# Kernel optimization log

Measured on AMD Instinct MI355X. Metric: run time of the kernel, lower is better.

Reference implementation:

```python
import jax, jax.numpy as jnp
import numpy as np

GAMMA = 1.0
T = 2.0
EPS = 1e-8

def setup_inputs() -> dict:
    key = jax.random.key(0)
    k1, k2 = jax.random.split(key)
    N, D = 8192, 64
    user_vecs = jax.random.normal(k1, (N, D), dtype=jnp.float32)
    item_vecs = jax.random.normal(k2, (N, D), dtype=jnp.float32)
    return {"user_vecs": user_vecs, "item_vecs": item_vecs}

def _normalize(x):
    return x / jnp.linalg.norm(x, axis=-1, keepdims=True)

def _alignment(u, i):
    u = _normalize(u)
    i = _normalize(i)
    return jnp.mean(jnp.sum((u - i) ** 2, axis=1))

def _uniformity(x):
    # log( mean_{i<j} exp(-t * ||x_i - x_j||^2) + eps ) with normalized x.
    # For unit vectors ||x_i - x_j||^2 = 2 - 2 <x_i, x_j>. Use full symmetric
    # Gram matrix: sum over off-diagonal = 2 * sum over i<j; diag contributes
    # exp(0) = 1 per row, so subtract N, divide by N*(N-1).
    x = _normalize(x)
    n = x.shape[0]
    gram = x @ x.T                       # [N, N]
    sq_pdist = jnp.maximum(2.0 - 2.0 * gram, 0.0)
    total = jnp.sum(jnp.exp(-T * sq_pdist))
    mean_pair = (total - n) / (n * (n - 1))
    return jnp.log(mean_pair + EPS)

def reference(user_vecs, item_vecs):
    align = _alignment(user_vecs, item_vecs)
    uniform = GAMMA * (_uniformity(user_vecs) + _uniformity(item_vecs)) / 2.0
    return align + uniform
```

## Files before the change

kernel.cpp:

```cpp
#include <hip/hip_runtime.h>
#include <cstdint>


#define NROWS 8192
#define DIM 64
#define NT2 32
#define GRAM_SLOTS (NT2 * (NT2 + 1))
#define K1_BLOCKS 512

static constexpr float SQRT_SCALE = 2.4022448309943147f;
static constexpr float E4        = 54.598150033144236f;
static constexpr float E4_INV    = 0.018315638888734179f;
static constexpr float EPS_F = 1e-8f;

typedef __bf16 bf16x8 __attribute__((ext_vector_type(8)));
typedef float f32x4 __attribute__((ext_vector_type(4)));

__device__ __forceinline__ unsigned short f32_to_bf16_rn(float f) {
    union { float f; uint32_t u; } c; c.f = f;
    uint32_t u = c.u;
    uint32_t r = u + 0x7FFFu + ((u >> 16) & 1u);
    return (unsigned short)(r >> 16);
}

__global__ void __launch_bounds__(256) normalize_align_kernel(
    const float* __restrict__ user, const float* __restrict__ item,
    unsigned short* __restrict__ xu, unsigned short* __restrict__ xi,
    float* __restrict__ pa, float* __restrict__ acc, unsigned* __restrict__ ctr)
{
    if (blockIdx.x == 0) {
        if (threadIdx.x < 16) acc[threadIdx.x] = 0.0f;
        else if (threadIdx.x == 16) *ctr = 0u;
    }

    const int wave = threadIdx.x >> 6;
    const int lane = threadIdx.x & 63;
    const int wid  = blockIdx.x * 4 + wave;

    float asum = 0.0f;
    #pragma unroll
    for (int r = 0; r < 4; ++r) {
        const int idx = (wid * 4 + r) * DIM + lane;
        float u = user[idx];
        float v = item[idx];
        float su = u * u, sv = v * v;
        #pragma unroll
        for (int m = 1; m < 64; m <<= 1) {
            su += __shfl_xor(su, m, 64);
            sv += __shfl_xor(sv, m, 64);
        }
        float iu = rsqrtf(su); iu = iu * (1.5f - 0.5f * su * iu * iu);
        float iv = rsqrtf(sv); iv = iv * (1.5f - 0.5f * sv * iv * iv);
        float un = u * iu, vn = v * iv;
        xu[idx] = f32_to_bf16_rn(un * SQRT_SCALE);
        xi[idx] = f32_to_bf16_rn(vn * SQRT_SCALE);
        float d = un - vn;
        asum += d * d;
    }
    #pragma unroll
    for (int m = 1; m < 64; m <<= 1) asum += __shfl_xor(asum, m, 64);
    __shared__ float ws4[4];
    if (lane == 0) ws4[wave] = asum;
    __syncthreads();
    if (threadIdx.x == 0) pa[blockIdx.x] = ws4[0] + ws4[1] + ws4[2] + ws4[3];
}

__global__ void __launch_bounds__(512, 8) gram_exp_kernel(
    const unsigned short* __restrict__ xu,
    const unsigned short* __restrict__ xi,
    const float* __restrict__ pa,
    float* __restrict__ acc, unsigned* __restrict__ ctr,
    float* __restrict__ out)
{
    const int bx = blockIdx.x, by = blockIdx.y;
    const unsigned short* __restrict__ X;
    int bi, bj;
    bool is_item;
    if (by < NT2) {
        if (by >= bx) { X = xu; bi = bx; bj = by; is_item = false; }
        else          { X = xi; bi = by; bj = bx; is_item = true;  }
    } else            { X = xi; bi = bx; bj = bx; is_item = true;  }
    const bool diag = (bi == bj);

    __shared__ unsigned short lds[16384];
    __shared__ float wsum[8];
    __shared__ float fin[16];
    __shared__ bool amLast;

    const int wave = threadIdx.x >> 6;
    const int lane = threadIdx.x & 63;

    bf16x8 a[2][2];
    {
        const int arow = bi * 256 + wave * 32 + (lane & 15);
        const int acol = (lane >> 4) * 8;
        #pragma unroll
        for (int rb = 0; rb < 2; ++rb)
            #pragma unroll
            for (int ks = 0; ks < 2; ++ks)
                a[rb][ks] = *reinterpret_cast<const bf16x8*>(
                    X + (arow + rb * 16) * DIM + acol + ks * 32);
    }

    {
        const int base = bj * 256;
        #pragma unroll
        for (int i = 0; i < 4; ++i) {
            int n = i * 512 + threadIdx.x;
            int r = n >> 3, c = n & 7;
            bf16x8 v = *reinterpret_cast<const bf16x8*>(X + (base + r) * DIM + c * 8);
            int di = (r >> 4) * 1024 + c * 128 + (r & 15) * 8;
            *reinterpret_cast<bf16x8*>(&lds[di]) = v;
        }
    }
    __syncthreads();

    float l0 = 0.0f, l1 = 0.0f;
    #pragma unroll 2
    for (int cb = 0; cb < 16; ++cb) {
        bf16x8 b0 = *reinterpret_cast<const bf16x8*>(&lds[cb * 1024 + lane * 8]);
        bf16x8 b1 = *reinterpret_cast<const bf16x8*>(&lds[cb * 1024 + 512 + lane * 8]);
        #pragma unroll
        for (int rb = 0; rb < 2; ++rb) {
            f32x4 c = {0.f, 0.f, 0.f, 0.f};
            c = __builtin_amdgcn_mfma_f32_16x16x32_bf16(a[rb][0], b0, c, 0, 0, 0);
            c = __builtin_amdgcn_mfma_f32_16x16x32_bf16(a[rb][1], b1, c, 0, 0, 0);
            #pragma unroll
            for (int e = 0; e < 4; ++e) {
                float ex = __builtin_amdgcn_exp2f(c[e]);
                if (diag) ex = fminf(ex, E4);
                if (e & 1) l1 += ex; else l0 += ex;
            }
        }
    }

    float local = l0 + l1;
    #pragma unroll
    for (int m = 1; m < 64; m <<= 1) local += __shfl_xor(local, m, 64);
    if (lane == 0) wsum[wave] = local;
    __syncthreads();
    if (threadIdx.x == 0) {
        float t = 0.f;
        #pragma unroll
        for (int w = 0; w < 8; ++w) t += wsum[w];
        t = diag ? t : 2.0f * t;
        atomicAdd(&acc[(is_item ? 8 : 0) + (bx & 7)], t);
        __threadfence();
        unsigned prev = atomicAdd(ctr, 1u);
        amLast = (prev == GRAM_SLOTS - 1);
    }
    __syncthreads();

    if (amLast) {
        __threadfence();
        float av = pa[threadIdx.x];
        #pragma unroll
        for (int m = 1; m < 64; m <<= 1) av += __shfl_xor(av, m, 64);
        if (lane == 0) wsum[wave] = av;
        if (threadIdx.x < 16)
            fin[threadIdx.x] = atomicAdd(&acc[threadIdx.x], 0.0f);
        __syncthreads();
        if (threadIdx.x == 0) {
            float A = 0.f;
            #pragma unroll
            for (int w = 0; w < 8; ++w) A += wsum[w];
            float su = 0.f, si = 0.f;
            #pragma unroll
            for (int s = 0; s < 8; ++s) { su += fin[s]; si += fin[8 + s]; }
            su *= E4_INV; si *= E4_INV;
            const float n = (float)NROWS;
            const float denom = n * (n - 1.0f);
            out[0] = A / n + 0.5f * (logf((su - n) / denom + EPS_F)
                                   + logf((si - n) / denom + EPS_F));
        }
    }
}

extern "C" void kernel_launch(void* const* d_in, const int* in_sizes, int n_in,
                              void* d_out, int out_size, void* d_ws, size_t ws_size,
                              hipStream_t stream)
{
    const float* user = (const float*)d_in[0];
    const float* item = (const float*)d_in[1];

    unsigned short* xu = (unsigned short*)d_ws;
    unsigned short* xi = xu + (size_t)NROWS * DIM;
    float* pa  = (float*)(xi + (size_t)NROWS * DIM);
    float* acc = pa + K1_BLOCKS;
    unsigned* ctr = (unsigned*)(acc + 16);

    normalize_align_kernel<<<K1_BLOCKS, 256, 0, stream>>>(user, item, xu, xi,
                                                          pa, acc, ctr);
    gram_exp_kernel<<<dim3(NT2, NT2 + 1), 512, 0, stream>>>(xu, xi, pa, acc,
                                                            ctr, (float*)d_out);
}
```

Baseline: 88.37 us.

## Split completion counter per row and pad accumulators to avoid atomic contention

```diff
diff --git a/kernel.cpp b/kernel.cpp
--- a/kernel.cpp
+++ b/kernel.cpp
@@ -5,13 +5,15 @@
 #define NROWS 8192
 #define DIM 64
 #define NT2 32
-#define GRAM_SLOTS (NT2 * (NT2 + 1))
 #define K1_BLOCKS 512
 
 static constexpr float SQRT_SCALE = 2.4022448309943147f;
 static constexpr float E4        = 54.598150033144236f;
 static constexpr float E4_INV    = 0.018315638888734179f;
 static constexpr float EPS_F = 1e-8f;
+
+#define NSLOTS 26
+#define SLOT_STRIDE 32
 
 typedef __bf16 bf16x8 __attribute__((ext_vector_type(8)));
 typedef float f32x4 __attribute__((ext_vector_type(4)));
@@ -26,11 +28,14 @@
 __global__ void __launch_bounds__(256) normalize_align_kernel(
     const float* __restrict__ user, const float* __restrict__ item,
     unsigned short* __restrict__ xu, unsigned short* __restrict__ xi,
-    float* __restrict__ pa, float* __restrict__ acc, unsigned* __restrict__ ctr)
+    float* __restrict__ pa, float* __restrict__ sums,
+    unsigned* __restrict__ ctrs, unsigned* __restrict__ master)
 {
     if (blockIdx.x == 0) {
-        if (threadIdx.x < 16) acc[threadIdx.x] = 0.0f;
-        else if (threadIdx.x == 16) *ctr = 0u;
+        const int t = threadIdx.x;
+        if (t < NSLOTS) sums[t * SLOT_STRIDE] = 0.0f;
+        else if (t >= 32 && t < 32 + NT2 + 1) ctrs[(t - 32) * SLOT_STRIDE] = 0u;
+        else if (t == 70) *master = 0u;
     }
 
     const int wave = threadIdx.x >> 6;
@@ -69,7 +74,8 @@
     const unsigned short* __restrict__ xu,
     const unsigned short* __restrict__ xi,
     const float* __restrict__ pa,
-    float* __restrict__ acc, unsigned* __restrict__ ctr,
+    float* __restrict__ sums,
+    unsigned* __restrict__ ctrs, unsigned* __restrict__ master,
     float* __restrict__ out)
 {
     const int bx = blockIdx.x, by = blockIdx.y;
@@ -84,7 +90,7 @@
 
     __shared__ unsigned short lds[16384];
     __shared__ float wsum[8];
-    __shared__ float fin[16];
+    __shared__ float fin[NSLOTS];
     __shared__ bool amLast;
 
     const int wave = threadIdx.x >> 6;
@@ -113,10 +119,17 @@
             *reinterpret_cast<bf16x8*>(&lds[di]) = v;
         }
     }
+
+    if (by == NT2 && wave == 0) {
+        float s = (lane < 16) ? pa[bx * 16 + lane] : 0.0f;
+        #pragma unroll
+        for (int m = 1; m < 16; m <<= 1) s += __shfl_xor(s, m, 16);
+        if (lane == 0) atomicAdd(&sums[(bx & 7) * SLOT_STRIDE], s);
+    }
     __syncthreads();
 
     float l0 = 0.0f, l1 = 0.0f;
-    #pragma unroll 2
+    #pragma unroll
     for (int cb = 0; cb < 16; ++cb) {
         bf16x8 b0 = *reinterpret_cast<const bf16x8*>(&lds[cb * 1024 + lane * 8]);
         bf16x8 b1 = *reinterpret_cast<const bf16x8*>(&lds[cb * 1024 + 512 + lane * 8]);
@@ -144,29 +157,32 @@
         #pragma unroll
         for (int w = 0; w < 8; ++w) t += wsum[w];
         t = diag ? t : 2.0f * t;
-        atomicAdd(&acc[(is_item ? 8 : 0) + (bx & 7)], t);
+        atomicAdd(&sums[(8 + (is_item ? 8 : 0) + (bx & 7)) * SLOT_STRIDE], t);
         __threadfence();
-        unsigned prev = atomicAdd(ctr, 1u);
-        amLast = (prev == GRAM_SLOTS - 1);
+        unsigned prev = atomicAdd(&ctrs[by * SLOT_STRIDE], 1u);
+        bool last = false;
+        if (prev == NT2 - 1) {
+            __threadfence();
+            unsigned p2 = atomicAdd(master, 1u);
+            last = (p2 == NT2);
+        }
+        amLast = last;
     }
     __syncthreads();
 
     if (amLast) {
         __threadfence();
-        float av = pa[threadIdx.x];
-        #pragma unroll
-        for (int m = 1; m < 64; m <<= 1) av += __shfl_xor(av, m, 64);
-        if (lane == 0) wsum[wave] = av;
-        if (threadIdx.x < 16)
-            fin[threadIdx.x] = atomicAdd(&acc[threadIdx.x], 0.0f);
+        if (threadIdx.x < NSLOTS)
+            fin[threadIdx.x] = atomicAdd(&sums[threadIdx.x * SLOT_STRIDE], 0.0f);
         __syncthreads();
         if (threadIdx.x == 0) {
-            float A = 0.f;
+            float A = 0.f, su = 0.f, si = 0.f;
             #pragma unroll
-            for (int w = 0; w < 8; ++w) A += wsum[w];
-            float su = 0.f, si = 0.f;
-            #pragma unroll
-            for (int s = 0; s < 8; ++s) { su += fin[s]; si += fin[8 + s]; }
+            for (int s = 0; s < 8; ++s) {
+                A  += fin[s];
+                su += fin[8 + s];
+                si += fin[16 + s];
+            }
             su *= E4_INV; si *= E4_INV;
             const float n = (float)NROWS;
             const float denom = n * (n - 1.0f);
@@ -185,12 +201,14 @@
 
     unsigned short* xu = (unsigned short*)d_ws;
     unsigned short* xi = xu + (size_t)NROWS * DIM;
-    float* pa  = (float*)(xi + (size_t)NROWS * DIM);
-    float* acc = pa + K1_BLOCKS;
-    unsigned* ctr = (unsigned*)(acc + 16);
+    float* pa   = (float*)(xi + (size_t)NROWS * DIM);
+    float* sums = pa + K1_BLOCKS;
+    unsigned* ctrs   = (unsigned*)(sums + NSLOTS * SLOT_STRIDE);
+    unsigned* master = ctrs + (NT2 + 1) * SLOT_STRIDE;
 
     normalize_align_kernel<<<K1_BLOCKS, 256, 0, stream>>>(user, item, xu, xi,
-                                                          pa, acc, ctr);
-    gram_exp_kernel<<<dim3(NT2, NT2 + 1), 512, 0, stream>>>(xu, xi, pa, acc,
-                                                            ctr, (float*)d_out);
-}
+                                                          pa, sums, ctrs, master);
+    gram_exp_kernel<<<dim3(NT2, NT2 + 1), 512, 0, stream>>>(xu, xi, pa, sums,
+                                                            ctrs, master,
+                                                            (float*)d_out);
+}
```

Result: no change. 86.65 us (-2.0%).
